# Kernel tuning notes

Hardware: AMD Instinct MI355X
Metric: run time of the kernel (lower is better)

The kernel has to match this reference:

```python
import jax, jax.numpy as jnp
import numpy as np

B, N, NPOINT, C = 4, 16384, 4096, 64
NSAMPLE = 32


def setup_inputs() -> dict:
    key = jax.random.key(0)
    k1, k2, k3 = jax.random.split(key, 3)
    xyz = jax.random.normal(k1, (B, N, 3), dtype=jnp.float32)
    new_xyz = jax.random.normal(k2, (B, NPOINT, 3), dtype=jnp.float32)
    features = jax.random.normal(k3, (B, C, N), dtype=jnp.float32)
    return {"xyz": xyz, "new_xyz": new_xyz, "features": features, "nsample": NSAMPLE}


def _knn_idx(new_xyz, xyz, k):
    # squared pairwise distances: (B, npoint, N)
    dists = jnp.sum((new_xyz[:, :, None, :] - xyz[:, None, :, :]) ** 2, axis=-1)
    # k smallest distances -> top_k on negated distances (fused top-k instead of full argsort)
    _, idx = jax.lax.top_k(-dists, k)  # (B, npoint, k) int32
    return idx


def reference(xyz, new_xyz, features, nsample):
    idx = _knn_idx(new_xyz, xyz, nsample)  # (B, npoint, nsample)

    # group xyz: (B, npoint, nsample, 3)
    grouped_xyz = jax.vmap(lambda pts, i: pts[i])(xyz, idx)
    # center on the query points and move coords to channel dim: (B, 3, npoint, nsample)
    grouped_xyz = grouped_xyz - new_xyz[:, :, None, :]
    grouped_xyz = jnp.transpose(grouped_xyz, (0, 3, 1, 2))

    # group features: (B, C, npoint, nsample)
    grouped_features = jax.vmap(lambda f, i: f[:, i])(features, idx)

    # use_xyz=True -> concat along channel dim: (B, 3 + C, npoint, nsample)
    new_features = jnp.concatenate([grouped_xyz, grouped_features], axis=1)
    return new_features
```

## Files before the change

### kernel.cpp

```cpp
#include <hip/hip_runtime.h>

#define NBATCH 4
#define NPTS   16384
#define NQ     4096
#define NCH    64
#define K      32
#define CHOUT  67

typedef float v2f __attribute__((ext_vector_type(2)));
typedef float v4f __attribute__((ext_vector_type(4)));
typedef int   v4i __attribute__((ext_vector_type(4)));

__device__ __forceinline__ v2f pk_add(v2f a, v2f b) {
    v2f d; asm("v_pk_add_f32 %0, %1, %2" : "=v"(d) : "v"(a), "v"(b)); return d;
}
__device__ __forceinline__ v2f pk_mul(v2f a, v2f b) {
    v2f d; asm("v_pk_mul_f32 %0, %1, %2" : "=v"(d) : "v"(a), "v"(b)); return d;
}
__device__ __forceinline__ v2f pk_fma(v2f a, v2f b, v2f c) {
    v2f d; asm("v_pk_fma_f32 %0, %1, %2, %3" : "=v"(d) : "v"(a), "v"(b), "v"(c)); return d;
}
__device__ __forceinline__ int dpp_shr1(int v) {
    return __builtin_amdgcn_update_dpp(v, v, 0x138, 0xf, 0xf, false);
}
__device__ __forceinline__ int sel_mask_i(unsigned long long m, int t, int f) {
    int d; asm("v_cndmask_b32 %0, %2, %1, %3" : "=v"(d) : "v"(t), "v"(f), "s"(m));
    return d;
}

constexpr int TILE = 1024;
constexpr int NT   = NPTS / TILE;
constexpr int QPW  = 2;
constexpr int QPB  = 8;

#define VW3 asm volatile("s_waitcnt vmcnt(3)" ::: "memory")
#define VW0 asm volatile("s_waitcnt vmcnt(0)" ::: "memory")
#define BAR __builtin_amdgcn_s_barrier()

__global__ __launch_bounds__(256) void knn_kernel(
    const float* __restrict__ xyz,
    const float* __restrict__ new_xyz,
    int*   __restrict__ out_idx,
    float* __restrict__ out)
{
    __shared__ __align__(16) float sb[3][TILE * 3];

    const int tid  = threadIdx.x;
    const int lane = tid & 63;
    const int wave = tid >> 6;
    const int b    = blockIdx.x >> 9;
    const int q0   = (blockIdx.x & 511) * QPB + wave * QPW;

    const float* xb = xyz + (size_t)b * NPTS * 3;
    const char* gbase = (const char*)xb + wave * 3072 + lane * 16;

    auto STAGE = [&](int buf, int t0) {
        const char* g = gbase + (size_t)t0 * 12;
        char* l = (char*)(&sb[buf][0]) + wave * 3072;
#define GLL(k) __builtin_amdgcn_global_load_lds( \
        (const __attribute__((address_space(1))) unsigned int*)(g + (k) * 1024), \
        (__attribute__((address_space(3))) unsigned int*)(l + (k) * 1024), \
        16, 0, 0)
        GLL(0); GLL(1); GLL(2);
#undef GLL
    };

    float nqx[QPW], nqy[QPW], nqz[QPW];
    v2f nqx2[QPW], nqy2[QPW], nqz2[QPW];
#pragma unroll
    for (int j = 0; j < QPW; ++j) {
        const int base = ((b * NQ) + q0 + j) * 3;
        nqx[j] = __int_as_float(__builtin_amdgcn_readfirstlane(__float_as_int(-new_xyz[base + 0])));
        nqy[j] = __int_as_float(__builtin_amdgcn_readfirstlane(__float_as_int(-new_xyz[base + 1])));
        nqz[j] = __int_as_float(__builtin_amdgcn_readfirstlane(__float_as_int(-new_xyz[base + 2])));
        nqx2[j] = (v2f){nqx[j], nqx[j]};
        nqy2[j] = (v2f){nqy[j], nqy[j]};
        nqz2[j] = (v2f){nqz[j], nqz[j]};
    }

    const float INF  = __int_as_float(0x7f800000);
    const float NINF = __int_as_float(0xff800000);

    float vmA[QPW], vmB[QPW];
#pragma unroll
    for (int j = 0; j < QPW; ++j) { vmA[j] = INF; vmB[j] = INF; }

    STAGE(0, 0);
    STAGE(1, TILE);
    VW3; BAR;
    {
        int cur = 0, pre = 2;
        for (int t = 0; t < NT; ++t) {
            if (t + 2 < NT) STAGE(pre, (t + 2) * TILE);
            const float* sp = &sb[cur][0];
#pragma unroll
            for (int ii = 0; ii < TILE / 128; ++ii) {
                const float* qp = sp + 3 * (ii * 128 + lane);
                const v2f px2 = {qp[0], qp[192]};
                const v2f py2 = {qp[1], qp[193]};
                const v2f pz2 = {qp[2], qp[194]};
#pragma unroll
                for (int j = 0; j < QPW; ++j) {
                    const v2f dx = pk_add(px2, nqx2[j]);
                    const v2f dy = pk_add(py2, nqy2[j]);
                    const v2f dz = pk_add(pz2, nqz2[j]);
                    const v2f d2 = pk_fma(dx, dx, pk_fma(dy, dy, pk_mul(dz, dz)));
                    vmA[j] = fminf(vmA[j], d2.x);
                    vmB[j] = fminf(vmB[j], d2.y);
                }
            }
            if (t + 1 < NT) {
                if (t + 2 < NT) { VW3; } else { VW0; }
                BAR;
            }
            cur = (cur == 2) ? 0 : cur + 1;
            pre = (pre == 2) ? 0 : pre + 1;
        }
    }
    BAR;

    STAGE(0, 0);
    STAGE(1, TILE);

    float Tf[QPW];
#pragma unroll
    for (int j = 0; j < QPW; ++j) {
        const unsigned u = __float_as_uint(fminf(vmA[j], vmB[j]));
        unsigned t = 0x7fffffffu;
        for (int bb = 30; bb >= 0; --bb) {
            const unsigned tt = t ^ (1u << bb);
            const int cnt = __popcll(__ballot(u <= tt));
            if (cnt >= 32) t = tt;
        }
        Tf[j] = __uint_as_float(t + 64);
    }

    float ld[QPW]; int li[QPW];
#pragma unroll
    for (int j = 0; j < QPW; ++j) {
        ld[j] = (lane < K) ? INF : NINF;
        li[j] = 0;
    }

    VW3; BAR;
    {
        int cur = 0, pre = 2;
        for (int t = 0; t < NT; ++t) {
            if (t + 2 < NT) STAGE(pre, (t + 2) * TILE);
            const int t0 = t * TILE;
            const float* sp = &sb[cur][0];
#pragma unroll
            for (int ii = 0; ii < TILE / 128; ++ii) {
                const int gb = t0 + ii * 128;
                const float* qp = sp + 3 * (ii * 128 + lane);
                const v2f px2 = {qp[0], qp[192]};
                const v2f py2 = {qp[1], qp[193]};
                const v2f pz2 = {qp[2], qp[194]};
#pragma unroll
                for (int j = 0; j < QPW; ++j) {
                    const v2f dx = pk_add(px2, nqx2[j]);
                    const v2f dy = pk_add(py2, nqy2[j]);
                    const v2f dz = pk_add(pz2, nqz2[j]);
                    const v2f d2 = pk_add(pk_add(pk_mul(dx, dx), pk_mul(dy, dy)),
                                          pk_mul(dz, dz));
                    unsigned long long m0 = __ballot(d2.x <= Tf[j]);
                    unsigned long long m1 = __ballot(d2.y <= Tf[j]);
                    while (m0 | m1) {
                        const bool lo = (m0 != 0);
                        const unsigned long long mm = lo ? m0 : m1;
                        const int c = (int)__builtin_ctzll(mm);
                        if (lo) m0 &= m0 - 1; else m1 &= m1 - 1;
                        const int b0 = __builtin_amdgcn_readlane(__float_as_int(d2.x), c);
                        const int b1 = __builtin_amdgcn_readlane(__float_as_int(d2.y), c);
                        const float dn = __int_as_float(lo ? b0 : b1);
                        const int cand = gb + (lo ? 0 : 64) + c;
                        const unsigned long long sh = __ballot(ld[j] > dn);
                        const int p = sh ? (int)__builtin_ctzll(sh) : 64;
                        const int sld = dpp_shr1(__float_as_int(ld[j]));
                        const int sli = dpp_shr1(li[j]);
                        const int nld = sel_mask_i(sh, sld, __float_as_int(ld[j]));
                        const int nli = sel_mask_i(sh, sli, li[j]);
                        ld[j] = __int_as_float((lane == p) ? __float_as_int(dn) : nld);
                        li[j] = (lane == p) ? cand : nli;
                    }
                }
            }
            if (t + 1 < NT) {
                if (t + 2 < NT) { VW3; } else { VW0; }
                BAR;
            }
            cur = (cur == 2) ? 0 : cur + 1;
            pre = (pre == 2) ? 0 : pre + 1;
        }
    }

#pragma unroll
    for (int j = 0; j < QPW; ++j) {
        if (lane < K) {
            const int q   = q0 + j;
            const int idx = li[j];
            out_idx[((size_t)(b * NQ) + q) * K + lane] = idx;
            const float px = xb[idx * 3 + 0];
            const float py = xb[idx * 3 + 1];
            const float pz = xb[idx * 3 + 2];
            const size_t plane = (size_t)NQ * K;
            const size_t o = (((size_t)b * CHOUT + 0) * NQ + q) * K + lane;
            out[o]             = __fadd_rn(px, nqx[j]);
            out[o + plane]     = __fadd_rn(py, nqy[j]);
            out[o + 2 * plane] = __fadd_rn(pz, nqz[j]);
        }
    }
}

__global__ __launch_bounds__(256) void transpose_kernel(
    const float* __restrict__ f, float* __restrict__ ft)
{
    __shared__ float sm[128][65];
    const int tid = threadIdx.x;
    const int nb  = blockIdx.x & (NPTS / 128 - 1);
    const int b   = blockIdx.x >> 7;
    const int n0  = nb * 128;
    const float* fb = f + (size_t)b * NCH * NPTS;
    const int nn = tid & 127, chh = tid >> 7;
#pragma unroll
    for (int c = 0; c < NCH; c += 2)
        sm[nn][c + chh] = fb[(size_t)(c + chh) * NPTS + n0 + nn];
    __syncthreads();
    float* ftb = ft + ((size_t)b * NPTS + n0) * NCH;
#pragma unroll
    for (int g = 0; g < 32; ++g) {
        const int o = g * 256 + tid;
        ftb[o] = sm[o >> 6][o & 63];
    }
}

__global__ __launch_bounds__(256) void gather2_kernel(
    const float* __restrict__ ft,
    const int*   __restrict__ idx,
    float* __restrict__ out)
{
    __shared__ float smc[NCH][129];

    const int tid = threadIdx.x;
    const int qt  = blockIdx.x & (NQ / 4 - 1);
    const int b   = blockIdx.x >> 10;
    const size_t slot0 = ((size_t)b * NQ + (size_t)qt * 4) * K;

    const int s = tid >> 1;
    const int h = tid & 1;
    const int p = idx[slot0 + s];
    const v4f* src = (const v4f*)(ft + ((size_t)b * NPTS + p) * NCH) + h * 8;
    v4f r[8];
#pragma unroll
    for (int k = 0; k < 8; ++k) r[k] = src[k];
#pragma unroll
    for (int k = 0; k < 8; ++k) {
        const int c0 = h * 32 + k * 4;
        smc[c0 + 0][s] = r[k].x;
        smc[c0 + 1][s] = r[k].y;
        smc[c0 + 2][s] = r[k].z;
        smc[c0 + 3][s] = r[k].w;
    }
    __syncthreads();

    const int w = tid >> 6, l = tid & 63;
    const size_t plane = (size_t)NQ * K;
    float* ob = out + ((size_t)b * CHOUT + 3) * plane + (size_t)qt * (4 * K);
#pragma unroll
    for (int c = w; c < NCH; c += 4) {
        float* orow = ob + (size_t)c * plane;
        orow[l]      = smc[c][l];
        orow[64 + l] = smc[c][64 + l];
    }
}

__global__ __launch_bounds__(1024) void gather_kernel(
    const float* __restrict__ features,
    const int*   __restrict__ idx,
    float* __restrict__ out)
{
    __shared__ __align__(16) float row[NPTS];

    const int tid  = threadIdx.x;
    const int half = blockIdx.x & 1;
    const int c    = (blockIdx.x >> 1) & 63;
    const int b    = blockIdx.x >> 7;

    const v4f* src = (const v4f*)(features + ((size_t)(b * NCH + c)) * NPTS);
    for (int k2 = tid; k2 < NPTS / 4; k2 += 1024) ((v4f*)row)[k2] = src[k2];
    __syncthreads();

    const size_t hofs = (size_t)half * (NQ * K / 2);
    const v4i* gi = (const v4i*)(idx + (size_t)b * NQ * K + hofs);
    v4f* dst = (v4f*)(out + ((size_t)(b * CHOUT + 3 + c)) * NQ * K + hofs);

    v4i cur = gi[tid];
#pragma unroll
    for (int it = 0; it < 16; ++it) {
        v4i nxt;
        if (it < 15) nxt = gi[tid + (it + 1) * 1024];
        v4f o;
        o.x = row[cur.x]; o.y = row[cur.y]; o.z = row[cur.z]; o.w = row[cur.w];
        dst[tid + it * 1024] = o;
        cur = nxt;
    }
}

extern "C" void kernel_launch(void* const* d_in, const int* in_sizes, int n_in,
                              void* d_out, int out_size, void* d_ws, size_t ws_size,
                              hipStream_t stream) {
    const float* xyz      = (const float*)d_in[0];
    const float* new_xyz  = (const float*)d_in[1];
    const float* features = (const float*)d_in[2];
    float* out    = (float*)d_out;
    int*   ws_idx = (int*)d_ws;

    const size_t idx_bytes = (size_t)NBATCH * NQ * K * sizeof(int);
    const size_t ft_bytes  = (size_t)NBATCH * NPTS * NCH * sizeof(float);
    float* featT = (float*)((char*)d_ws + idx_bytes);

    if (ws_size >= idx_bytes + ft_bytes) {
        transpose_kernel<<<dim3(NBATCH * (NPTS / 128)), dim3(256), 0, stream>>>(features, featT);
        knn_kernel<<<dim3(NBATCH * (NQ / QPB)), dim3(256), 0, stream>>>(xyz, new_xyz, ws_idx, out);
        gather2_kernel<<<dim3(NBATCH * (NQ / 4)), dim3(256), 0, stream>>>(featT, ws_idx, out);
    } else {
        knn_kernel<<<dim3(NBATCH * (NQ / QPB)), dim3(256), 0, stream>>>(xyz, new_xyz, ws_idx, out);
        gather_kernel<<<dim3(NBATCH * NCH * 2), dim3(1024), 0, stream>>>(features, ws_idx, out);
    }
}
```

Baseline: 338.1 us.

## Fuse feature gather into KNN kernel and double queries per wave

Moves the feature gather from the separate gather2 kernel into the KNN kernel's epilogue, so each wave reads the transposed feature rows for its own neighbours and writes them straight to the output. This drops one kernel launch and the round trip of neighbour indices through global memory. Queries per wave go from 2 to 4, which halves the number of xyz tile loads per query but raises register pressure and halves the grid size. The fused stores are no longer staged through LDS, so each lane writes one float per channel plane, which may coalesce less well than before.

```diff
diff --git a/kernel.cpp b/kernel.cpp
--- a/kernel.cpp
+++ b/kernel.cpp
@@ -30,16 +30,18 @@
 
 constexpr int TILE = 1024;
 constexpr int NT   = NPTS / TILE;
-constexpr int QPW  = 2;
-constexpr int QPB  = 8;
+constexpr int QPW  = 4;
+constexpr int QPB  = 16;
 
 #define VW3 asm volatile("s_waitcnt vmcnt(3)" ::: "memory")
 #define VW0 asm volatile("s_waitcnt vmcnt(0)" ::: "memory")
 #define BAR __builtin_amdgcn_s_barrier()
 
+template <bool FUSED>
 __global__ __launch_bounds__(256) void knn_kernel(
     const float* __restrict__ xyz,
     const float* __restrict__ new_xyz,
+    const float* __restrict__ ft,
     int*   __restrict__ out_idx,
     float* __restrict__ out)
 {
@@ -48,8 +50,8 @@
     const int tid  = threadIdx.x;
     const int lane = tid & 63;
     const int wave = tid >> 6;
-    const int b    = blockIdx.x >> 9;
-    const int q0   = (blockIdx.x & 511) * QPB + wave * QPW;
+    const int b    = blockIdx.x >> 8;
+    const int q0   = (blockIdx.x & 255) * QPB + wave * QPW;
 
     const float* xb = xyz + (size_t)b * NPTS * 3;
     const char* gbase = (const char*)xb + wave * 3072 + lane * 16;
@@ -194,20 +196,38 @@
         }
     }
 
+    const size_t plane = (size_t)NQ * K;
 #pragma unroll
     for (int j = 0; j < QPW; ++j) {
+        const int q = q0 + j;
         if (lane < K) {
-            const int q   = q0 + j;
             const int idx = li[j];
-            out_idx[((size_t)(b * NQ) + q) * K + lane] = idx;
             const float px = xb[idx * 3 + 0];
             const float py = xb[idx * 3 + 1];
             const float pz = xb[idx * 3 + 2];
-            const size_t plane = (size_t)NQ * K;
             const size_t o = (((size_t)b * CHOUT + 0) * NQ + q) * K + lane;
             out[o]             = __fadd_rn(px, nqx[j]);
             out[o + plane]     = __fadd_rn(py, nqy[j]);
             out[o + 2 * plane] = __fadd_rn(pz, nqz[j]);
+        }
+        if (FUSED) {
+            const int s = lane & 31, h = lane >> 5;
+            const int pidx = __shfl(li[j], s);
+            const v4f* src = (const v4f*)(ft + ((size_t)b * NPTS + pidx) * NCH) + h * 8;
+            v4f r[8];
+#pragma unroll
+            for (int k2 = 0; k2 < 8; ++k2) r[k2] = src[k2];
+            float* ob = out + (((size_t)b * CHOUT + 3) * NQ + q) * K + s;
+#pragma unroll
+            for (int k2 = 0; k2 < 8; ++k2) {
+                const int c0 = h * 32 + k2 * 4;
+                ob[(size_t)(c0 + 0) * plane] = r[k2].x;
+                ob[(size_t)(c0 + 1) * plane] = r[k2].y;
+                ob[(size_t)(c0 + 2) * plane] = r[k2].z;
+                ob[(size_t)(c0 + 3) * plane] = r[k2].w;
+            }
+        } else if (lane < K) {
+            out_idx[((size_t)(b * NQ) + q) * K + lane] = li[j];
         }
     }
 }
@@ -234,46 +254,6 @@
     }
 }
 
-__global__ __launch_bounds__(256) void gather2_kernel(
-    const float* __restrict__ ft,
-    const int*   __restrict__ idx,
-    float* __restrict__ out)
-{
-    __shared__ float smc[NCH][129];
-
-    const int tid = threadIdx.x;
-    const int qt  = blockIdx.x & (NQ / 4 - 1);
-    const int b   = blockIdx.x >> 10;
-    const size_t slot0 = ((size_t)b * NQ + (size_t)qt * 4) * K;
-
-    const int s = tid >> 1;
-    const int h = tid & 1;
-    const int p = idx[slot0 + s];
-    const v4f* src = (const v4f*)(ft + ((size_t)b * NPTS + p) * NCH) + h * 8;
-    v4f r[8];
-#pragma unroll
-    for (int k = 0; k < 8; ++k) r[k] = src[k];
-#pragma unroll
-    for (int k = 0; k < 8; ++k) {
-        const int c0 = h * 32 + k * 4;
-        smc[c0 + 0][s] = r[k].x;
-        smc[c0 + 1][s] = r[k].y;
-        smc[c0 + 2][s] = r[k].z;
-        smc[c0 + 3][s] = r[k].w;
-    }
-    __syncthreads();
-
-    const int w = tid >> 6, l = tid & 63;
-    const size_t plane = (size_t)NQ * K;
-    float* ob = out + ((size_t)b * CHOUT + 3) * plane + (size_t)qt * (4 * K);
-#pragma unroll
-    for (int c = w; c < NCH; c += 4) {
-        float* orow = ob + (size_t)c * plane;
-        orow[l]      = smc[c][l];
-        orow[64 + l] = smc[c][64 + l];
-    }
-}
-
 __global__ __launch_bounds__(1024) void gather_kernel(
     const float* __restrict__ features,
     const int*   __restrict__ idx,
@@ -312,19 +292,19 @@
     const float* xyz      = (const float*)d_in[0];
     const float* new_xyz  = (const float*)d_in[1];
     const float* features = (const float*)d_in[2];
-    float* out    = (float*)d_out;
-    int*   ws_idx = (int*)d_ws;
-
-    const size_t idx_bytes = (size_t)NBATCH * NQ * K * sizeof(int);
-    const size_t ft_bytes  = (size_t)NBATCH * NPTS * NCH * sizeof(float);
-    float* featT = (float*)((char*)d_ws + idx_bytes);
-
-    if (ws_size >= idx_bytes + ft_bytes) {
+    float* out = (float*)d_out;
+
+    const size_t ft_bytes = (size_t)NBATCH * NPTS * NCH * sizeof(float);
+
+    if (ws_size >= ft_bytes) {
+        float* featT = (float*)d_ws;
         transpose_kernel<<<dim3(NBATCH * (NPTS / 128)), dim3(256), 0, stream>>>(features, featT);
-        knn_kernel<<<dim3(NBATCH * (NQ / QPB)), dim3(256), 0, stream>>>(xyz, new_xyz, ws_idx, out);
-        gather2_kernel<<<dim3(NBATCH * (NQ / 4)), dim3(256), 0, stream>>>(featT, ws_idx, out);
+        knn_kernel<true><<<dim3(NBATCH * (NQ / QPB)), dim3(256), 0, stream>>>(
+            xyz, new_xyz, featT, nullptr, out);
     } else {
-        knn_kernel<<<dim3(NBATCH * (NQ / QPB)), dim3(256), 0, stream>>>(xyz, new_xyz, ws_idx, out);
+        int* ws_idx = (int*)d_ws;
+        knn_kernel<false><<<dim3(NBATCH * (NQ / QPB)), dim3(256), 0, stream>>>(
+            xyz, new_xyz, nullptr, ws_idx, out);
         gather_kernel<<<dim3(NBATCH * NCH * 2), dim3(1024), 0, stream>>>(features, ws_idx, out);
     }
 }
```

After: 291.5 us. 1.16x faster.
